# Optimization experiments

Hardware: AMD Instinct MI355X
Metric: run time of the kernel (lower is better)

## Reference

```python
import jax, jax.numpy as jnp
import numpy as np

NEG = -1e9

def _leaky(x, slope):
    return jnp.where(x >= 0, x, slope * x)

def _mlp_sig(x, w1, b1, w2, b2):
    # Linear -> LeakyReLU(0.01) -> Linear -> Sigmoid  (a graph_discover expert)
    return jax.nn.sigmoid(_leaky(x @ w1 + b1, 0.01) @ w2 + b2)

def _gatv2(x, adj, wl, bl, wr, br, we, att, bias):
    # Dense-masked GATv2Conv (PyG semantics): edge s->t exists iff adj[b,s,t] != 0,
    # edge_attr is the adjacency value (edge_dim=1), heads concatenated.
    B, Np, _ = x.shape
    heads, out_ch = att.shape
    xl = (x @ wl + bl).reshape(B, Np, heads, out_ch)  # source transform (messages)
    xr = (x @ wr + br).reshape(B, Np, heads, out_ch)  # target transform
    adjT = jnp.swapaxes(adj, 1, 2)                    # [b, target, source]
    ea = adjT[..., None, None] * we.reshape(heads, out_ch)   # lin_edge (no bias)
    e = _leaky(xl[:, None, :, :, :] + xr[:, :, None, :, :] + ea, 0.2)  # (B,T,S,H,O)
    logits = jnp.einsum('btsho,ho->btsh', e, att)
    m = adjT != 0
    logits = jnp.where(m[..., None], logits, NEG)
    alpha = jax.nn.softmax(logits, axis=2) * m[..., None]    # zero rows with no in-edges
    out = jnp.einsum('btsh,bsho->btho', alpha, xl)
    return out.reshape(B, Np, heads * out_ch) + bias

def _forward(latent, gumbel_noise,
             d0_w1, d0_b1, d0_w2, d0_b2,
             d1_w1, d1_b1, d1_w2, d1_b2,
             a_w, a_b,
             g1_wl, g1_bl, g1_wr, g1_br, g1_we, g1_att, g1_bias,
             g2_wl, g2_bl, g2_wr, g2_br, g2_we, g2_att, g2_bias):
    B, C, Hh, Ww = latent.shape
    N = Hh * Ww
    lat = jnp.transpose(latent, (0, 2, 3, 1)).reshape(B, N, C)
    # positional encoding (dropout = identity in eval)
    pos = jnp.arange(N, dtype=jnp.float32)[:, None]
    div = jnp.exp(jnp.arange(0, C, 2, dtype=jnp.float32) * (-np.log(10000.0) / C))
    pe = jnp.zeros((N, C), lat.dtype).at[:, 0::2].set(jnp.sin(pos * div)).at[:, 1::2].set(jnp.cos(pos * div))
    pl = lat + pe
    mask = jnp.zeros((B, N, 1), lat.dtype)  # forward() hardcodes mask = 0

    # pairwise node concat: inp[b, i*N+j] = [pl[b,i], pl[b,j]]
    ni = jnp.repeat(pl, N, axis=1)
    nj = jnp.tile(pl, (1, N, 1))
    inp = jnp.concatenate([ni, nj], axis=-1)  # (B, N*N, 2C)
    no_inter = _mlp_sig(inp, d0_w1, d0_b1, d0_w2, d0_b2).reshape(B, N, N)
    # action = zeros -> argmax = 0 for every row -> all rows routed to expert graph_discovers[1]
    inter = _mlp_sig(inp, d1_w1, d1_b1, d1_w2, d1_b2).reshape(B, N, N)
    adj = no_inter * (1 - mask) + inter * mask

    # differentiable Bernoulli via hard gumbel-softmax (straight-through)
    logits = jnp.log(jnp.clip(jnp.stack([1 - adj, adj], axis=-1), 1e-4))
    y = jax.nn.softmax(logits + gumbel_noise, axis=-1)
    y_hard = jax.nn.one_hot(jnp.argmax(y, axis=-1), 2, dtype=y.dtype)
    cg = (y_hard + y - jax.lax.stop_gradient(y))[..., 1]
    weighted = adj * cg

    # _compute_y, noise='off': append action node, pad adjacency (right col = 1, bottom row = 0)
    action = jnp.zeros((B, a_w.shape[0]), lat.dtype)
    action_node = action @ a_w + a_b
    nodes = jnp.concatenate([pl, action_node[:, None, :]], axis=1)  # (B, N+1, C)
    adj_p = jnp.pad(weighted, ((0, 0), (0, 0), (0, 1)), constant_values=1.0)
    adj_p = jnp.pad(adj_p, ((0, 0), (0, 1), (0, 0)), constant_values=0.0)

    x1 = _leaky(_gatv2(nodes, adj_p, g1_wl, g1_bl, g1_wr, g1_br, g1_we, g1_att, g1_bias), 0.01)
    x2 = _gatv2(x1, adj_p, g2_wl, g2_bl, g2_wr, g2_br, g2_we, g2_att, g2_bias)  # (B, N+1, heads*C)
    ny = x2[:, :N, :]
    # action argmax = 0 -> gathered head is columns [C, 2C)
    out = ny[..., :C] * (1 - mask) + ny[..., C:2 * C] * mask
    return jax.nn.softmax(out, axis=-1)

def setup_inputs() -> dict:
    key = jax.random.key(0)
    ks = jax.random.split(key, 32)
    B, C, Hh, Ww = 4, 64, 14, 14
    N = Hh * Ww
    A = 4
    heads = 1 + A
    D0, O1 = 800, 100
    f32 = jnp.float32
    def nrm(k, shp, sc=0.05):
        return jax.random.normal(k, shp, f32) * sc
    return {
        'latent': jax.random.normal(ks[0], (B, C, Hh, Ww), f32),
        'gumbel_noise': jax.random.gumbel(ks[1], (B, N, N, 2), f32),
        'd0_w1': nrm(ks[2], (2 * C, D0)), 'd0_b1': jnp.zeros((D0,), f32),
        'd0_w2': nrm(ks[3], (D0, 1)), 'd0_b2': jnp.zeros((1,), f32),
        'd1_w1': nrm(ks[4], (2 * C, D0)), 'd1_b1': jnp.zeros((D0,), f32),
        'd1_w2': nrm(ks[5], (D0, 1)), 'd1_b2': jnp.zeros((1,), f32),
        'a_w': nrm(ks[6], (A, C)), 'a_b': nrm(ks[7], (C,)),
        'g1_wl': nrm(ks[8], (C, heads * O1)), 'g1_bl': jnp.zeros((heads * O1,), f32),
        'g1_wr': nrm(ks[9], (C, heads * O1)), 'g1_br': jnp.zeros((heads * O1,), f32),
        'g1_we': nrm(ks[10], (heads * O1,)), 'g1_att': nrm(ks[11], (heads, O1)),
        'g1_bias': jnp.zeros((heads * O1,), f32),
        'g2_wl': nrm(ks[12], (heads * O1, heads * C)), 'g2_bl': jnp.zeros((heads * C,), f32),
        'g2_wr': nrm(ks[13], (heads * O1, heads * C)), 'g2_br': jnp.zeros((heads * C,), f32),
        'g2_we': nrm(ks[14], (heads * C,)), 'g2_att': nrm(ks[15], (heads, C)),
        'g2_bias': jnp.zeros((heads * C,), f32),
    }

def reference(latent, gumbel_noise,
              d0_w1, d0_b1, d0_w2, d0_b2,
              d1_w1, d1_b1, d1_w2, d1_b2,
              a_w, a_b,
              g1_wl, g1_bl, g1_wr, g1_br, g1_we, g1_att, g1_bias,
              g2_wl, g2_bl, g2_wr, g2_br, g2_we, g2_att, g2_bias):
    return _forward(latent, gumbel_noise,
                    d0_w1, d0_b1, d0_w2, d0_b2,
                    d1_w1, d1_b1, d1_w2, d1_b2,
                    a_w, a_b,
                    g1_wl, g1_bl, g1_wr, g1_br, g1_we, g1_att, g1_bias,
                    g2_wl, g2_bl, g2_wr, g2_br, g2_we, g2_att, g2_bias)
```

## Files before the change

kernel.cpp:

```cpp
#include <hip/hip_runtime.h>
#include <math.h>

#define NB 4
#define NN 196
#define NC 64
#define ND0 800
#define NH 5
#define NO1 100
#define NC1 500
#define NO2 64
#define TT 2
#define JC 4
#define JW 200
#define RT 7
#define RW 2
#define NEGF -1000000000.0f
#define TH_MARGIN 0.002f

__global__ void __launch_bounds__(256)
k_head(const float* __restrict__ latent,
       const float* __restrict__ w1, const float* __restrict__ b1,
       const float* __restrict__ wl, const float* __restrict__ bl,
       const float* __restrict__ wr, const float* __restrict__ br,
       double* __restrict__ U_d, double* __restrict__ V_d,
       float* __restrict__ U_f, float* __restrict__ VT_f,
       float* __restrict__ xl1, float* __restrict__ xl1T, float* __restrict__ xr1,
       int* __restrict__ bcount) {
    __shared__ double rowd[RT][NC];
    __shared__ float  rowf[RW][NC];
    int bi = blockIdx.x;
    int tid = threadIdx.x;
    if (bi == 0 && tid == 0) *bcount = 0;
    const int NUV = NB*(NN/RT)*4;
    if (bi < NUV) {
        int b = bi / ((NN/RT)*4);
        int rem = bi % ((NN/RT)*4);
        int tile = rem >> 2;
        int q = rem & 3;
        int n0 = tile * RT;
        for (int idx = tid; idx < RT*NC; idx += 256) {
            int r = idx >> 6, c = idx & 63;
            int n = n0 + r;
            double div = exp((double)(2*(c >> 1)) * (-log(10000.0) / (double)NC));
            double ang = (double)n * div;
            double pe = (c & 1) ? cos(ang) : sin(ang);
            rowd[r][c] = (double)latent[(b*NC + c)*NN + n] + pe;
        }
        __syncthreads();
        int j = q*200 + tid;
        if (tid < 200) {
            double au[RT], av[RT];
            double bb = (double)b1[j];
            #pragma unroll
            for (int r = 0; r < RT; ++r) { au[r] = 0.0; av[r] = bb; }
            #pragma unroll 4
            for (int k = 0; k < NC; ++k) {
                double wu = (double)w1[k*ND0 + j];
                double wv = (double)w1[(NC + k)*ND0 + j];
                #pragma unroll
                for (int r = 0; r < RT; ++r) {
                    au[r] += rowd[r][k] * wu;
                    av[r] += rowd[r][k] * wv;
                }
            }
            size_t bn0 = (size_t)(b*NN + n0);
            #pragma unroll
            for (int r = 0; r < RT; ++r) {
                U_d[(bn0 + r)*ND0 + j] = au[r];
                V_d[(bn0 + r)*ND0 + j] = av[r];
                U_f[(bn0 + r)*ND0 + j] = (float)au[r];
                VT_f[((size_t)b*ND0 + j)*NN + n0 + r] = (float)av[r];
            }
        }
    } else {
        int bn2 = bi - NUV;
        int b = bn2 / (NN/RW);
        int n0 = (bn2 % (NN/RW)) * RW;
        for (int idx = tid; idx < RW*NC; idx += 256) {
            int r = idx >> 6, c = idx & 63;
            int n = n0 + r;
            double div = exp((double)(2*(c >> 1)) * (-log(10000.0) / (double)NC));
            double ang = (double)n * div;
            double pe = (c & 1) ? cos(ang) : sin(ang);
            rowf[r][c] = (float)((double)latent[(b*NC + c)*NN + n] + pe);
        }
        __syncthreads();
        for (int c = tid; c < NC1; c += 256) {
            float al0 = bl[c], ar0 = br[c];
            float al1 = al0, ar1 = ar0;
            #pragma unroll 8
            for (int k = 0; k < NC; ++k) {
                float wlk = wl[k*NC1 + c];
                float wrk = wr[k*NC1 + c];
                float p0 = rowf[0][k], p1 = rowf[1][k];
                al0 += p0 * wlk; al1 += p1 * wlk;
                ar0 += p0 * wrk; ar1 += p1 * wrk;
            }
            size_t bn0 = (size_t)(b*NN + n0);
            xl1[bn0*NC1 + c] = al0;
            xl1[(bn0 + 1)*NC1 + c] = al1;
            xr1[bn0*NC1 + c] = ar0;
            xr1[(bn0 + 1)*NC1 + c] = ar1;
            xl1T[((size_t)b*NC1 + c)*256 + n0] = al0;
            xl1T[((size_t)b*NC1 + c)*256 + n0 + 1] = al1;
        }
    }
}

__global__ void __launch_bounds__(1024)
k_adj32(const float* __restrict__ U_f, const float* __restrict__ VT,
        const float* __restrict__ w2, const float* __restrict__ b2,
        const float* __restrict__ gum, float* __restrict__ WT,
        int* __restrict__ blist, int* __restrict__ bcount) {
    __shared__ float Ul[TT][ND0];
    __shared__ float w2l[ND0];
    __shared__ float part[JC][TT][256];
    int bi = blockIdx.x;
    int b = bi / (NN/TT);
    int t0 = (bi % (NN/TT)) * TT;
    int tid = threadIdx.x;
    int s = tid & 255;
    int chunk = tid >> 8;
    for (int idx = tid; idx < TT*ND0; idx += 1024) {
        int tt = idx / ND0, j = idx - tt*ND0;
        Ul[tt][j] = U_f[((size_t)(b*NN + t0 + tt))*ND0 + j];
    }
    for (int j = tid; j < ND0; j += 1024) w2l[j] = w2[j];
    __syncthreads();
    float a0 = 0.0f, a1 = 0.0f;
    if (s < NN) {
        const float* vp = VT + ((size_t)b*ND0 + chunk*JW)*NN + s;
        int j0 = chunk*JW;
        #pragma unroll 4
        for (int jj = 0; jj < JW; ++jj) {
            float v = vp[(size_t)jj*NN];
            float w = w2l[j0 + jj];
            float h0 = Ul[0][j0 + jj] + v; h0 = (h0 >= 0.0f) ? h0 : 0.01f*h0; a0 = fmaf(h0, w, a0);
            float h1 = Ul[1][j0 + jj] + v; h1 = (h1 >= 0.0f) ? h1 : 0.01f*h1; a1 = fmaf(h1, w, a1);
        }
    }
    part[chunk][0][s] = a0;
    part[chunk][1][s] = a1;
    __syncthreads();
    if (tid < TT*NN) {
        int tt = tid / NN, ss = tid - tt*NN;
        float acc = b2[0] + part[0][tt][ss] + part[1][tt][ss]
                  + part[2][tt][ss] + part[3][tt][ss];
        int t = t0 + tt;
        float adj = 1.0f/(1.0f + expf(-acc));
        float l1 = logf(fmaxf(adj, 1e-4f));
        float l0 = logf(fmaxf(1.0f - adj, 1e-4f));
        float g0 = gum[((size_t)(b*NN + t)*NN + ss)*2 + 0];
        float g1 = gum[((size_t)(b*NN + t)*NN + ss)*2 + 1];
        float margin = (l1 + g1) - (l0 + g0);
        if (fabsf(margin) <= TH_MARGIN) {
            int li = atomicAdd(bcount, 1);
            blist[li] = (b*NN + t)*NN + ss;
        }
        WT[((size_t)(b*NN + ss))*NN + t] = (margin > 0.0f) ? adj : 0.0f;
    }
}

__global__ void __launch_bounds__(256)
k_adjfix(const double* __restrict__ U, const double* __restrict__ V,
         const float* __restrict__ w2, const float* __restrict__ b2,
         const float* __restrict__ gum, const int* __restrict__ blist,
         const int* __restrict__ bcount, float* __restrict__ WT) {
    int nfix = *bcount;
    int gwid = (blockIdx.x * blockDim.x + threadIdx.x) >> 6;
    int lane = threadIdx.x & 63;
    int nw = (gridDim.x * blockDim.x) >> 6;
    for (int i = gwid; i < nfix; i += nw) {
        int code = blist[i];
        int s = code % NN;
        int t = (code / NN) % NN;
        int b = code / (NN*NN);
        const double* up = U + ((size_t)(b*NN + t))*ND0;
        const double* vp = V + ((size_t)(b*NN + s))*ND0;
        double a = 0.0;
        for (int j = lane; j < ND0; j += 64) {
            double h = up[j] + vp[j];
            h = (h >= 0.0) ? h : 0.01*h;
            a += h * (double)w2[j];
        }
        for (int off = 32; off >= 1; off >>= 1) a += __shfl_xor(a, off);
        if (lane == 0) {
            double acc = a + (double)b2[0];
            double adj = 1.0/(1.0 + exp(-acc));
            double l1 = log(fmax(adj, 1e-4));
            double l0 = log(fmax(1.0 - adj, 1e-4));
            double g0 = (double)gum[((size_t)(b*NN + t)*NN + s)*2 + 0];
            double g1 = (double)gum[((size_t)(b*NN + t)*NN + s)*2 + 1];
            double z0 = l0 + g0, z1 = l1 + g1;
            double m = fmax(z0, z1);
            double e0 = exp(z0 - m), e1 = exp(z1 - m);
            double sm = e0 + e1;
            int cg = (e1/sm) > (e0/sm);
            WT[((size_t)(b*NN + s))*NN + t] = cg ? (float)adj : 0.0f;
        }
    }
}

__global__ void __launch_bounds__(256)
k_gat1a(const float* __restrict__ xl1T, const float* __restrict__ xr1,
        const float* __restrict__ WT, const float* __restrict__ we,
        const float* __restrict__ att, float* __restrict__ alphaG) {
    __shared__ float wred[4][2];
    __shared__ float mxs[2], sms[2];
    int blk = blockIdx.x;
    int tp = blk % (NN/2);
    int bh = blk / (NN/2);
    int h = bh % NH;
    int b = bh / NH;
    int t0 = tp*2;
    int s = threadIdx.x;
    int lane = s & 63, wid = s >> 6;
    float wt0 = (s < NN) ? WT[((size_t)(b*NN + t0))*NN + s] : 0.0f;
    float wt1 = (s < NN) ? WT[((size_t)(b*NN + t0 + 1))*NN + s] : 0.0f;
    const float* xT  = xl1T + ((size_t)b*NC1 + h*NO1)*256;
    const float* xr0 = xr1 + ((size_t)(b*NN + t0))*NC1 + h*NO1;
    const float* xr1p= xr1 + ((size_t)(b*NN + t0 + 1))*NC1 + h*NO1;
    const float* weh = we + h*NO1;
    const float* ath = att + h*NO1;
    float a0 = 0.0f, a1 = 0.0f;
    #pragma unroll 5
    for (int o = 0; o < NO1; ++o) {
        float x = xT[(size_t)o*256 + s];
        float w = weh[o];
        float av = ath[o];
        float av2 = 0.2f*av;
        float v0 = fmaf(wt0, w, x + xr0[o]);
        float v1 = fmaf(wt1, w, x + xr1p[o]);
        a0 += fmaxf(v0, 0.0f)*av + fminf(v0, 0.0f)*av2;
        a1 += fmaxf(v1, 0.0f)*av + fminf(v1, 0.0f)*av2;
    }
    bool on0 = (s < NN) && (wt0 != 0.0f);
    bool on1 = (s < NN) && (wt1 != 0.0f);
    float m0 = on0 ? a0 : NEGF;
    float m1 = on1 ? a1 : NEGF;
    #pragma unroll
    for (int off = 32; off >= 1; off >>= 1) {
        m0 = fmaxf(m0, __shfl_xor(m0, off));
        m1 = fmaxf(m1, __shfl_xor(m1, off));
    }
    if (lane == 0) { wred[wid][0] = m0; wred[wid][1] = m1; }
    __syncthreads();
    if (s < 2) mxs[s] = fmaxf(fmaxf(wred[0][s], wred[1][s]), fmaxf(wred[2][s], wred[3][s]));
    __syncthreads();
    float e0 = on0 ? expf(a0 - mxs[0]) : 0.0f;
    float e1 = on1 ? expf(a1 - mxs[1]) : 0.0f;
    float r0 = e0, r1 = e1;
    #pragma unroll
    for (int off = 32; off >= 1; off >>= 1) {
        r0 += __shfl_xor(r0, off);
        r1 += __shfl_xor(r1, off);
    }
    if (lane == 0) { wred[wid][0] = r0; wred[wid][1] = r1; }
    __syncthreads();
    if (s < 2) sms[s] = wred[0][s] + wred[1][s] + wred[2][s] + wred[3][s];
    __syncthreads();
    alphaG[((size_t)bh*NN + t0)*256 + s]     = (sms[0] > 0.0f) ? e0 / sms[0] : 0.0f;
    alphaG[((size_t)bh*NN + t0 + 1)*256 + s] = (sms[1] > 0.0f) ? e1 / sms[1] : 0.0f;
}

__global__ void __launch_bounds__(640)
k_gat1bp(const float* __restrict__ xl1, const float* __restrict__ alphaG,
         const float* __restrict__ bias,
         const float* __restrict__ wl2, const float* __restrict__ bl2,
         const float* __restrict__ wr2, const float* __restrict__ br2,
         float* __restrict__ xl2, float* __restrict__ xl2T, float* __restrict__ xr2) {
    __shared__ float row[2][NC1 + 4];
    __shared__ float part[2][2][5][NO2];
    int blk = blockIdx.x;
    int b = blk / (NN/2), tp = blk % (NN/2);
    int t0 = tp*2;
    int tid = threadIdx.x;
    int w = tid >> 6, l = tid & 63;
    int h = w >> 1, csub = w & 1;
    int o = csub*64 + l;
    bool active = (o < NO1);
    int c = h*NO1 + (active ? o : 0);
    const float* ap = alphaG + (((size_t)b*NH + h)*NN + t0)*256;
    const float* xp = xl1 + (size_t)b*NN*NC1 + c;
    float a0 = 0.f, a1 = 0.f;
    for (int s = 0; s < NN; ++s) {
        float x = xp[(size_t)s*NC1];
        a0 = fmaf(ap[s], x, a0);
        a1 = fmaf(ap[256 + s], x, a1);
    }
    if (active) {
        float bs = bias[c];
        float v0 = a0 + bs; row[0][c] = (v0 >= 0.f) ? v0 : 0.01f*v0;
        float v1 = a1 + bs; row[1][c] = (v1 >= 0.f) ? v1 : 0.01f*v1;
    }
    __syncthreads();
    int which = tid / 320;
    int t5 = tid - which*320;
    int seg = t5 >> 6;
    int oo = t5 & 63;
    const float* wmat = which ? wr2 : wl2;
    float p0 = 0.f, p1 = 0.f;
    for (int k = seg*100; k < seg*100 + 100; ++k) {
        float wv = wmat[(size_t)k*320 + oo];
        p0 = fmaf(row[0][k], wv, p0);
        p1 = fmaf(row[1][k], wv, p1);
    }
    part[0][which][seg][oo] = p0;
    part[1][which][seg][oo] = p1;
    __syncthreads();
    if (tid < 256) {
        int r = tid >> 7;
        int wh = (tid >> 6) & 1;
        int o2 = tid & 63;
        float tot = part[r][wh][0][o2] + part[r][wh][1][o2] + part[r][wh][2][o2]
                  + part[r][wh][3][o2] + part[r][wh][4][o2];
        int n = t0 + r;
        size_t bn = (size_t)(b*NN + n);
        if (wh == 0) {
            float vv = tot + bl2[o2];
            xl2[bn*NO2 + o2] = vv;
            xl2T[((size_t)b*NO2 + o2)*256 + n] = vv;
        } else {
            xr2[bn*NO2 + o2] = tot + br2[o2];
        }
    }
}

__global__ void __launch_bounds__(256)
k_gat2(const float* __restrict__ xl2T, const float* __restrict__ xl2,
       const float* __restrict__ xr2, const float* __restrict__ WT,
       const float* __restrict__ we, const float* __restrict__ att,
       const float* __restrict__ bias, float* __restrict__ out) {
    __shared__ float red[256], alpha_l[256], part[4][NO2];
    __shared__ float mxs, sms;
    int blk = blockIdx.x;
    int b = blk / NN, t = blk % NN;
    int s = threadIdx.x;
    float wt = (s < NN) ? WT[((size_t)(b*NN + t))*NN + s] : 0.0f;
    const float* xT = xl2T + (size_t)b*NO2*256;
    const float* xr = xr2 + ((size_t)(b*NN + t))*NO2;
    float acc = 0.0f;
    for (int c = 0; c < NO2; ++c) {
        float x = xT[(size_t)c*256 + s];
        float v = fmaf(wt, we[c], x + xr[c]);
        float av = att[c];
        acc += fmaxf(v, 0.0f)*av + fminf(v, 0.0f)*(0.2f*av);
    }
    bool on = (s < NN) && (wt != 0.0f);
    float lgt = on ? acc : NEGF;
    red[s] = lgt;
    __syncthreads();
    for (int d = 128; d >= 1; d >>= 1) {
        if (s < d) red[s] = fmaxf(red[s], red[s + d]);
        __syncthreads();
    }
    if (s == 0) mxs = red[0];
    __syncthreads();
    float e = on ? expf(acc - mxs) : 0.0f;
    red[s] = e;
    __syncthreads();
    for (int d = 128; d >= 1; d >>= 1) {
        if (s < d) red[s] += red[s + d];
        __syncthreads();
    }
    if (s == 0) sms = red[0];
    __syncthreads();
    alpha_l[s] = (sms > 0.0f) ? e / sms : 0.0f;
    __syncthreads();
    int c = s & 63, sq = s >> 6;
    float pa = 0.0f;
    const float* xp = xl2 + (size_t)b*NN*NO2 + c;
    for (int ss = sq*49; ss < sq*49 + 49; ++ss)
        pa = fmaf(alpha_l[ss], xp[(size_t)ss*NO2], pa);
    part[sq][c] = pa;
    __syncthreads();
    if (s < NO2) {
        float ny = part[0][s] + part[1][s] + part[2][s] + part[3][s] + bias[s];
        float m = ny;
        for (int off = 32; off >= 1; off >>= 1) m = fmaxf(m, __shfl_xor(m, off));
        float ee = expf(ny - m);
        float ssum = ee;
        for (int off = 32; off >= 1; off >>= 1) ssum += __shfl_xor(ssum, off);
        out[((size_t)(b*NN + t))*NO2 + s] = ee / ssum;
    }
}

extern "C" void kernel_launch(void* const* d_in, const int* in_sizes, int n_in,
                              void* d_out, int out_size, void* d_ws, size_t ws_size,
                              hipStream_t stream) {
    const float* latent  = (const float*)d_in[0];
    const float* gum     = (const float*)d_in[1];
    const float* d0_w1   = (const float*)d_in[2];
    const float* d0_b1   = (const float*)d_in[3];
    const float* d0_w2   = (const float*)d_in[4];
    const float* d0_b2   = (const float*)d_in[5];
    const float* g1_wl   = (const float*)d_in[12];
    const float* g1_bl   = (const float*)d_in[13];
    const float* g1_wr   = (const float*)d_in[14];
    const float* g1_br   = (const float*)d_in[15];
    const float* g1_we   = (const float*)d_in[16];
    const float* g1_att  = (const float*)d_in[17];
    const float* g1_bias = (const float*)d_in[18];
    const float* g2_wl   = (const float*)d_in[19];
    const float* g2_bl   = (const float*)d_in[20];
    const float* g2_wr   = (const float*)d_in[21];
    const float* g2_br   = (const float*)d_in[22];
    const float* g2_we   = (const float*)d_in[23];
    const float* g2_att  = (const float*)d_in[24];
    const float* g2_bias = (const float*)d_in[25];
    float* out = (float*)d_out;

    char* ws = (char*)d_ws;
    size_t off = 0;
    auto alloc = [&](size_t bytes) { char* p = ws + off; off += (bytes + 255) & ~(size_t)255; return (void*)p; };
    double* U_d   = (double*)alloc((size_t)NB*NN*ND0*8);
    double* V_d   = (double*)alloc((size_t)NB*NN*ND0*8);
    float*  U_f   = (float*) alloc((size_t)NB*NN*ND0*4);
    float*  VT_f  = (float*) alloc((size_t)NB*ND0*NN*4);
    float*  WT    = (float*) alloc((size_t)NB*NN*NN*4);
    float*  xl1   = (float*) alloc((size_t)NB*NN*NC1*4);
    float*  xl1T  = (float*) alloc((size_t)NB*NC1*256*4);
    float*  xr1   = (float*) alloc((size_t)NB*NN*NC1*4);
    float*  alphaG= (float*) alloc((size_t)NB*NH*NN*256*4);
    float*  xl2   = (float*) alloc((size_t)NB*NN*NO2*4);
    float*  xl2T  = (float*) alloc((size_t)NB*NO2*256*4);
    float*  xr2   = (float*) alloc((size_t)NB*NN*NO2*4);
    int*    blist = (int*)   alloc((size_t)NB*NN*NN*4);
    int*    bcount= (int*)   alloc(256);

    hipLaunchKernelGGL(k_head,   dim3(NB*(NN/RT)*4 + NB*(NN/RW)), dim3(256), 0, stream,
                       latent, d0_w1, d0_b1, g1_wl, g1_bl, g1_wr, g1_br,
                       U_d, V_d, U_f, VT_f, xl1, xl1T, xr1, bcount);
    hipLaunchKernelGGL(k_adj32,  dim3(NB*(NN/TT)),     dim3(1024), 0, stream, U_f, VT_f, d0_w2, d0_b2, gum, WT, blist, bcount);
    hipLaunchKernelGGL(k_adjfix, dim3(256),            dim3(256),  0, stream, U_d, V_d, d0_w2, d0_b2, gum, blist, bcount, WT);
    hipLaunchKernelGGL(k_gat1a,  dim3(NB*NH*(NN/2)),   dim3(256),  0, stream, xl1T, xr1, WT, g1_we, g1_att, alphaG);
    hipLaunchKernelGGL(k_gat1bp, dim3(NB*(NN/2)),      dim3(640),  0, stream, xl1, alphaG, g1_bias,
                       g2_wl, g2_bl, g2_wr, g2_br, xl2, xl2T, xr2);
    hipLaunchKernelGGL(k_gat2,   dim3(NB*NN),          dim3(256),  0, stream, xl2T, xl2, xr2, WT, g2_we, g2_att, g2_bias, out);
}
```

Baseline: 132.9 us.

## Fuse borderline-margin fixup into adjacency kernel and enlarge per-block row tiles

The double-precision recheck of near-tie gumbel decisions moves into the k_adj32 kernel through a shared-memory list. This removes the separate k_adjfix launch, the global atomic counter and the blist buffer. The float copy U_f is dropped, and k_adj32 instead converts U_d to float on load. k_head processes more rows per block (RT 14, RW 4) and k_gat1a handles 4 target rows per block, trading more registers per thread for fewer blocks and more reuse of the loaded weights.

Measured after the change: 151.4 us. 13.9% more time.

```diff
diff --git a/kernel.cpp b/kernel.cpp
--- a/kernel.cpp
+++ b/kernel.cpp
@@ -12,8 +12,9 @@
 #define TT 2
 #define JC 4
 #define JW 200
-#define RT 7
-#define RW 2
+#define RT 14
+#define RW 4
+#define TG 4
 #define NEGF -1000000000.0f
 #define TH_MARGIN 0.002f
 
@@ -23,14 +24,12 @@
        const float* __restrict__ wl, const float* __restrict__ bl,
        const float* __restrict__ wr, const float* __restrict__ br,
        double* __restrict__ U_d, double* __restrict__ V_d,
-       float* __restrict__ U_f, float* __restrict__ VT_f,
-       float* __restrict__ xl1, float* __restrict__ xl1T, float* __restrict__ xr1,
-       int* __restrict__ bcount) {
+       float* __restrict__ VT_f,
+       float* __restrict__ xl1, float* __restrict__ xl1T, float* __restrict__ xr1) {
     __shared__ double rowd[RT][NC];
     __shared__ float  rowf[RW][NC];
     int bi = blockIdx.x;
     int tid = threadIdx.x;
-    if (bi == 0 && tid == 0) *bcount = 0;
     const int NUV = NB*(NN/RT)*4;
     if (bi < NUV) {
         int b = bi / ((NN/RT)*4);
@@ -53,7 +52,7 @@
             double bb = (double)b1[j];
             #pragma unroll
             for (int r = 0; r < RT; ++r) { au[r] = 0.0; av[r] = bb; }
-            #pragma unroll 4
+            #pragma unroll 2
             for (int k = 0; k < NC; ++k) {
                 double wu = (double)w1[k*ND0 + j];
                 double wv = (double)w1[(NC + k)*ND0 + j];
@@ -68,7 +67,6 @@
             for (int r = 0; r < RT; ++r) {
                 U_d[(bn0 + r)*ND0 + j] = au[r];
                 V_d[(bn0 + r)*ND0 + j] = av[r];
-                U_f[(bn0 + r)*ND0 + j] = (float)au[r];
                 VT_f[((size_t)b*ND0 + j)*NN + n0 + r] = (float)av[r];
             }
         }
@@ -76,8 +74,8 @@
         int bn2 = bi - NUV;
         int b = bn2 / (NN/RW);
         int n0 = (bn2 % (NN/RW)) * RW;
-        for (int idx = tid; idx < RW*NC; idx += 256) {
-            int r = idx >> 6, c = idx & 63;
+        {
+            int r = tid >> 6, c = tid & 63;
             int n = n0 + r;
             double div = exp((double)(2*(c >> 1)) * (-log(10000.0) / (double)NC));
             double ang = (double)n * div;
@@ -86,44 +84,51 @@
         }
         __syncthreads();
         for (int c = tid; c < NC1; c += 256) {
-            float al0 = bl[c], ar0 = br[c];
-            float al1 = al0, ar1 = ar0;
+            float al[RW], ar[RW];
+            float blc = bl[c], brc = br[c];
+            #pragma unroll
+            for (int r = 0; r < RW; ++r) { al[r] = blc; ar[r] = brc; }
             #pragma unroll 8
             for (int k = 0; k < NC; ++k) {
                 float wlk = wl[k*NC1 + c];
                 float wrk = wr[k*NC1 + c];
-                float p0 = rowf[0][k], p1 = rowf[1][k];
-                al0 += p0 * wlk; al1 += p1 * wlk;
-                ar0 += p0 * wrk; ar1 += p1 * wrk;
+                #pragma unroll
+                for (int r = 0; r < RW; ++r) {
+                    al[r] += rowf[r][k] * wlk;
+                    ar[r] += rowf[r][k] * wrk;
+                }
             }
             size_t bn0 = (size_t)(b*NN + n0);
-            xl1[bn0*NC1 + c] = al0;
-            xl1[(bn0 + 1)*NC1 + c] = al1;
-            xr1[bn0*NC1 + c] = ar0;
-            xr1[(bn0 + 1)*NC1 + c] = ar1;
-            xl1T[((size_t)b*NC1 + c)*256 + n0] = al0;
-            xl1T[((size_t)b*NC1 + c)*256 + n0 + 1] = al1;
+            #pragma unroll
+            for (int r = 0; r < RW; ++r) {
+                xl1[(bn0 + r)*NC1 + c] = al[r];
+                xr1[(bn0 + r)*NC1 + c] = ar[r];
+                xl1T[((size_t)b*NC1 + c)*256 + n0 + r] = al[r];
+            }
         }
     }
 }
 
 __global__ void __launch_bounds__(1024)
-k_adj32(const float* __restrict__ U_f, const float* __restrict__ VT,
+k_adj32(const double* __restrict__ U_d, const float* __restrict__ VT,
         const float* __restrict__ w2, const float* __restrict__ b2,
-        const float* __restrict__ gum, float* __restrict__ WT,
-        int* __restrict__ blist, int* __restrict__ bcount) {
+        const float* __restrict__ gum, const double* __restrict__ V_d,
+        float* __restrict__ WT) {
     __shared__ float Ul[TT][ND0];
     __shared__ float w2l[ND0];
     __shared__ float part[JC][TT][256];
+    __shared__ int   lcount;
+    __shared__ int   lpairs[TT*NN];
     int bi = blockIdx.x;
     int b = bi / (NN/TT);
     int t0 = (bi % (NN/TT)) * TT;
     int tid = threadIdx.x;
     int s = tid & 255;
     int chunk = tid >> 8;
+    if (tid == 0) lcount = 0;
     for (int idx = tid; idx < TT*ND0; idx += 1024) {
         int tt = idx / ND0, j = idx - tt*ND0;
-        Ul[tt][j] = U_f[((size_t)(b*NN + t0 + tt))*ND0 + j];
+        Ul[tt][j] = (float)U_d[((size_t)(b*NN + t0 + tt))*ND0 + j];
     }
     for (int j = tid; j < ND0; j += 1024) w2l[j] = w2[j];
     __syncthreads();
@@ -154,34 +159,25 @@
         float g1 = gum[((size_t)(b*NN + t)*NN + ss)*2 + 1];
         float margin = (l1 + g1) - (l0 + g0);
         if (fabsf(margin) <= TH_MARGIN) {
-            int li = atomicAdd(bcount, 1);
-            blist[li] = (b*NN + t)*NN + ss;
+            int li = atomicAdd(&lcount, 1);
+            lpairs[li] = (tt << 8) | ss;
         }
         WT[((size_t)(b*NN + ss))*NN + t] = (margin > 0.0f) ? adj : 0.0f;
     }
-}
-
-__global__ void __launch_bounds__(256)
-k_adjfix(const double* __restrict__ U, const double* __restrict__ V,
-         const float* __restrict__ w2, const float* __restrict__ b2,
-         const float* __restrict__ gum, const int* __restrict__ blist,
-         const int* __restrict__ bcount, float* __restrict__ WT) {
-    int nfix = *bcount;
-    int gwid = (blockIdx.x * blockDim.x + threadIdx.x) >> 6;
-    int lane = threadIdx.x & 63;
-    int nw = (gridDim.x * blockDim.x) >> 6;
-    for (int i = gwid; i < nfix; i += nw) {
-        int code = blist[i];
-        int s = code % NN;
-        int t = (code / NN) % NN;
-        int b = code / (NN*NN);
-        const double* up = U + ((size_t)(b*NN + t))*ND0;
-        const double* vp = V + ((size_t)(b*NN + s))*ND0;
+    __syncthreads();
+    int nfx = lcount;
+    int wid = tid >> 6, lane = tid & 63;
+    for (int i = wid; i < nfx; i += 16) {
+        int code = lpairs[i];
+        int tt = code >> 8, ss = code & 255;
+        int t = t0 + tt;
+        const double* up = U_d + ((size_t)(b*NN + t))*ND0;
+        const double* vp = V_d + ((size_t)(b*NN + ss))*ND0;
         double a = 0.0;
         for (int j = lane; j < ND0; j += 64) {
             double h = up[j] + vp[j];
             h = (h >= 0.0) ? h : 0.01*h;
-            a += h * (double)w2[j];
+            a += h * (double)w2l[j];
         }
         for (int off = 32; off >= 1; off >>= 1) a += __shfl_xor(a, off);
         if (lane == 0) {
@@ -189,14 +185,14 @@
             double adj = 1.0/(1.0 + exp(-acc));
             double l1 = log(fmax(adj, 1e-4));
             double l0 = log(fmax(1.0 - adj, 1e-4));
-            double g0 = (double)gum[((size_t)(b*NN + t)*NN + s)*2 + 0];
-            double g1 = (double)gum[((size_t)(b*NN + t)*NN + s)*2 + 1];
+            double g0 = (double)gum[((size_t)(b*NN + t)*NN + ss)*2 + 0];
+            double g1 = (double)gum[((size_t)(b*NN + t)*NN + ss)*2 + 1];
             double z0 = l0 + g0, z1 = l1 + g1;
             double m = fmax(z0, z1);
             double e0 = exp(z0 - m), e1 = exp(z1 - m);
             double sm = e0 + e1;
             int cg = (e1/sm) > (e0/sm);
-            WT[((size_t)(b*NN + s))*NN + t] = cg ? (float)adj : 0.0f;
+            WT[((size_t)(b*NN + ss))*NN + t] = cg ? (float)adj : 0.0f;
         }
     }
 }
@@ -205,62 +201,79 @@
 k_gat1a(const float* __restrict__ xl1T, const float* __restrict__ xr1,
         const float* __restrict__ WT, const float* __restrict__ we,
         const float* __restrict__ att, float* __restrict__ alphaG) {
-    __shared__ float wred[4][2];
-    __shared__ float mxs[2], sms[2];
+    __shared__ float wred[4][TG];
+    __shared__ float mxs[TG], sms[TG];
     int blk = blockIdx.x;
-    int tp = blk % (NN/2);
-    int bh = blk / (NN/2);
+    int tq = blk % (NN/TG);
+    int bh = blk / (NN/TG);
     int h = bh % NH;
     int b = bh / NH;
-    int t0 = tp*2;
+    int t0 = tq*TG;
     int s = threadIdx.x;
     int lane = s & 63, wid = s >> 6;
-    float wt0 = (s < NN) ? WT[((size_t)(b*NN + t0))*NN + s] : 0.0f;
-    float wt1 = (s < NN) ? WT[((size_t)(b*NN + t0 + 1))*NN + s] : 0.0f;
+    float wt[TG];
+    const float* xrp[TG];
+    #pragma unroll
+    for (int r = 0; r < TG; ++r) {
+        wt[r] = (s < NN) ? WT[((size_t)(b*NN + t0 + r))*NN + s] : 0.0f;
+        xrp[r] = xr1 + ((size_t)(b*NN + t0 + r))*NC1 + h*NO1;
+    }
     const float* xT  = xl1T + ((size_t)b*NC1 + h*NO1)*256;
-    const float* xr0 = xr1 + ((size_t)(b*NN + t0))*NC1 + h*NO1;
-    const float* xr1p= xr1 + ((size_t)(b*NN + t0 + 1))*NC1 + h*NO1;
     const float* weh = we + h*NO1;
     const float* ath = att + h*NO1;
-    float a0 = 0.0f, a1 = 0.0f;
+    float a[TG] = {0.f, 0.f, 0.f, 0.f};
     #pragma unroll 5
     for (int o = 0; o < NO1; ++o) {
         float x = xT[(size_t)o*256 + s];
         float w = weh[o];
         float av = ath[o];
         float av2 = 0.2f*av;
-        float v0 = fmaf(wt0, w, x + xr0[o]);
-        float v1 = fmaf(wt1, w, x + xr1p[o]);
-        a0 += fmaxf(v0, 0.0f)*av + fminf(v0, 0.0f)*av2;
-        a1 += fmaxf(v1, 0.0f)*av + fminf(v1, 0.0f)*av2;
-    }
-    bool on0 = (s < NN) && (wt0 != 0.0f);
-    bool on1 = (s < NN) && (wt1 != 0.0f);
-    float m0 = on0 ? a0 : NEGF;
-    float m1 = on1 ? a1 : NEGF;
+        #pragma unroll
+        for (int r = 0; r < TG; ++r) {
+            float v = fmaf(wt[r], w, x + xrp[r][o]);
+            a[r] += fmaxf(v, 0.0f)*av + fminf(v, 0.0f)*av2;
+        }
+    }
+    bool on[TG];
+    float m[TG];
+    #pragma unroll
+    for (int r = 0; r < TG; ++r) {
+        on[r] = (s < NN) && (wt[r] != 0.0f);
+        m[r] = on[r] ? a[r] : NEGF;
+    }
     #pragma unroll
     for (int off = 32; off >= 1; off >>= 1) {
-        m0 = fmaxf(m0, __shfl_xor(m0, off));
-        m1 = fmaxf(m1, __shfl_xor(m1, off));
-    }
-    if (lane == 0) { wred[wid][0] = m0; wred[wid][1] = m1; }
-    __syncthreads();
-    if (s < 2) mxs[s] = fmaxf(fmaxf(wred[0][s], wred[1][s]), fmaxf(wred[2][s], wred[3][s]));
-    __syncthreads();
-    float e0 = on0 ? expf(a0 - mxs[0]) : 0.0f;
-    float e1 = on1 ? expf(a1 - mxs[1]) : 0.0f;
-    float r0 = e0, r1 = e1;
+        #pragma unroll
+        for (int r = 0; r < TG; ++r) m[r] = fmaxf(m[r], __shfl_xor(m[r], off));
+    }
+    if (lane == 0) {
+        #pragma unroll
+        for (int r = 0; r < TG; ++r) wred[wid][r] = m[r];
+    }
+    __syncthreads();
+    if (s < TG) mxs[s] = fmaxf(fmaxf(wred[0][s], wred[1][s]), fmaxf(wred[2][s], wred[3][s]));
+    __syncthreads();
+    float e[TG], rr[TG];
+    #pragma unroll
+    for (int r = 0; r < TG; ++r) {
+        e[r] = on[r] ? expf(a[r] - mxs[r]) : 0.0f;
+        rr[r] = e[r];
+    }
     #pragma unroll
     for (int off = 32; off >= 1; off >>= 1) {
-        r0 += __shfl_xor(r0, off);
-        r1 += __shfl_xor(r1, off);
-    }
-    if (lane == 0) { wred[wid][0] = r0; wred[wid][1] = r1; }
-    __syncthreads();
-    if (s < 2) sms[s] = wred[0][s] + wred[1][s] + wred[2][s] + wred[3][s];
-    __syncthreads();
-    alphaG[((size_t)bh*NN + t0)*256 + s]     = (sms[0] > 0.0f) ? e0 / sms[0] : 0.0f;
-    alphaG[((size_t)bh*NN + t0 + 1)*256 + s] = (sms[1] > 0.0f) ? e1 / sms[1] : 0.0f;
+        #pragma unroll
+        for (int r = 0; r < TG; ++r) rr[r] += __shfl_xor(rr[r], off);
+    }
+    if (lane == 0) {
+        #pragma unroll
+        for (int r = 0; r < TG; ++r) wred[wid][r] = rr[r];
+    }
+    __syncthreads();
+    if (s < TG) sms[s] = wred[0][s] + wred[1][s] + wred[2][s] + wred[3][s];
+    __syncthreads();
+    #pragma unroll
+    for (int r = 0; r < TG; ++r)
+        alphaG[((size_t)bh*NN + t0 + r)*256 + s] = (sms[r] > 0.0f) ? e[r] / sms[r] : 0.0f;
 }
 
 __global__ void __launch_bounds__(640)
@@ -415,7 +428,6 @@
     auto alloc = [&](size_t bytes) { char* p = ws + off; off += (bytes + 255) & ~(size_t)255; return (void*)p; };
     double* U_d   = (double*)alloc((size_t)NB*NN*ND0*8);
     double* V_d   = (double*)alloc((size_t)NB*NN*ND0*8);
-    float*  U_f   = (float*) alloc((size_t)NB*NN*ND0*4);
     float*  VT_f  = (float*) alloc((size_t)NB*ND0*NN*4);
     float*  WT    = (float*) alloc((size_t)NB*NN*NN*4);
     float*  xl1   = (float*) alloc((size_t)NB*NN*NC1*4);
@@ -425,15 +437,13 @@
     float*  xl2   = (float*) alloc((size_t)NB*NN*NO2*4);
     float*  xl2T  = (float*) alloc((size_t)NB*NO2*256*4);
     float*  xr2   = (float*) alloc((size_t)NB*NN*NO2*4);
-    int*    blist = (int*)   alloc((size_t)NB*NN*NN*4);
-    int*    bcount= (int*)   alloc(256);
 
     hipLaunchKernelGGL(k_head,   dim3(NB*(NN/RT)*4 + NB*(NN/RW)), dim3(256), 0, stream,
                        latent, d0_w1, d0_b1, g1_wl, g1_bl, g1_wr, g1_br,
-                       U_d, V_d, U_f, VT_f, xl1, xl1T, xr1, bcount);
-    hipLaunchKernelGGL(k_adj32,  dim3(NB*(NN/TT)),     dim3(1024), 0, stream, U_f, VT_f, d0_w2, d0_b2, gum, WT, blist, bcount);
-    hipLaunchKernelGGL(k_adjfix, dim3(256),            dim3(256),  0, stream, U_d, V_d, d0_w2, d0_b2, gum, blist, bcount, WT);
-    hipLaunchKernelGGL(k_gat1a,  dim3(NB*NH*(NN/2)),   dim3(256),  0, stream, xl1T, xr1, WT, g1_we, g1_att, alphaG);
+                       U_d, V_d, VT_f, xl1, xl1T, xr1);
+    hipLaunchKernelGGL(k_adj32,  dim3(NB*(NN/TT)),     dim3(1024), 0, stream,
+                       U_d, VT_f, d0_w2, d0_b2, gum, V_d, WT);
+    hipLaunchKernelGGL(k_gat1a,  dim3(NB*NH*(NN/TG)),  dim3(256),  0, stream, xl1T, xr1, WT, g1_we, g1_att, alphaG);
     hipLaunchKernelGGL(k_gat1bp, dim3(NB*(NN/2)),      dim3(640),  0, stream, xl1, alphaG, g1_bias,
                        g2_wl, g2_bl, g2_wr, g2_br, xl2, xl2T, xr2);
     hipLaunchKernelGGL(k_gat2,   dim3(NB*NN),          dim3(256),  0, stream, xl2T, xl2, xr2, WT, g2_we, g2_att, g2_bias, out);
```
